# Optimization experiments

Measured on AMD Instinct MI355X. Metric: run time of the kernel, lower is better.

The kernel has to match this reference:

```python
import jax, jax.numpy as jnp
import numpy as np

N = 50000
E = 800000
IN_DIM = 512
H1 = IN_DIM // 2   # 256
H2 = IN_DIM // 4   # 128
D = 8
NP_CAYLEY = D * (D - 1) // 2  # 28


def setup_inputs() -> dict:
    key = jax.random.key(0)
    ks = jax.random.split(key, 10)
    x = jax.random.normal(ks[0], (N, IN_DIM), dtype=jnp.float32)
    edge_index = jax.random.randint(ks[1], (2, E), 0, N, dtype=jnp.int64)
    s1 = 1.0 / np.sqrt(IN_DIM)
    s2 = 1.0 / np.sqrt(H1)
    s3 = 1.0 / np.sqrt(H2)
    W1l = jax.random.uniform(ks[2], (H1, IN_DIM), jnp.float32, -s1, s1)
    b1 = jax.random.uniform(ks[3], (H1,), jnp.float32, -s1, s1)
    W1r = jax.random.uniform(ks[4], (H1, IN_DIM), jnp.float32, -s1, s1)
    W2l = jax.random.uniform(ks[5], (H2, H1), jnp.float32, -s2, s2)
    b2 = jax.random.uniform(ks[6], (H2,), jnp.float32, -s2, s2)
    W2r = jax.random.uniform(ks[7], (H2, H1), jnp.float32, -s2, s2)
    Wp = jax.random.uniform(ks[8], (NP_CAYLEY, H2), jnp.float32, -s3, s3)
    bp = jax.random.uniform(ks[9], (NP_CAYLEY,), jnp.float32, -s3, s3)
    return {"x": x, "edge_index": edge_index,
            "W1l": W1l, "b1": b1, "W1r": W1r,
            "W2l": W2l, "b2": b2, "W2r": W2r,
            "Wp": Wp, "bp": bp}


def _sage_conv(x, src, dst, Wl, bl, Wr):
    # PyG SAGEConv (mean aggr): out = lin_l(mean_{j in N(i)} x_j) + lin_r(x_i)
    msg_sum = jax.ops.segment_sum(x[src], dst, num_segments=N)  # [N, F]
    deg = jax.ops.segment_sum(jnp.ones((src.shape[0],), x.dtype), dst,
                              num_segments=N)
    mean = msg_sum / jnp.maximum(deg, 1.0)[:, None]
    return mean @ Wl.T + bl + x @ Wr.T


def _cayley(params):
    # params: [N, d(d-1)/2] -> skew A, then O = (I - A)^{-1} (I + A)
    iu, ju = jnp.triu_indices(D, k=1)  # row-major i<j matches torch loop order
    n = params.shape[0]
    A = jnp.zeros((n, D, D), params.dtype)
    A = A.at[:, iu, ju].set(params)
    A = A.at[:, ju, iu].set(-params)
    I = jnp.eye(D, dtype=params.dtype)
    return jnp.linalg.solve(I[None] - A, I[None] + A)


def reference(x, edge_index, W1l, b1, W1r, W2l, b2, W2r, Wp, bp):
    src, dst = edge_index[0], edge_index[1]
    h = jax.nn.relu(_sage_conv(x, src, dst, W1l, b1, W1r))
    h = jax.nn.relu(_sage_conv(h, src, dst, W2l, b2, W2r))
    params = h @ Wp.T + bp  # [N, 28]
    return _cayley(params)  # [N, 8, 8]
```

## Files before the change

### kernel.cpp

```cpp
#include <hip/hip_runtime.h>
#include <hip/hip_bf16.h>


#define WS_ALIGN(x) (((x) + 255) & ~size_t(255))

typedef __attribute__((ext_vector_type(8))) short short8;
typedef __attribute__((ext_vector_type(4))) float floatx4;

static __device__ __forceinline__ ushort f2b(float f) {
    unsigned u = __builtin_bit_cast(unsigned, f);
    u = (u + 0x7fffu + ((u >> 16) & 1u)) >> 16;
    return (ushort)u;
}
static __device__ __forceinline__ float b2f(ushort h) {
    unsigned u = ((unsigned)h) << 16;
    return __builtin_bit_cast(float, u);
}
static __device__ __forceinline__ unsigned pk2(float a, float b) {
    return (unsigned)f2b(a) | ((unsigned)f2b(b) << 16);
}


__global__ void hist_kernel(const int* __restrict__ dst, int* __restrict__ deg, int E) {
    int e = blockIdx.x * blockDim.x + threadIdx.x;
    if (e < E) atomicAdd(&deg[dst[e]], 1);
}

__global__ __launch_bounds__(256)
void scan_phase1(const int* __restrict__ deg, int* __restrict__ bsum, int n) {
    __shared__ int red[256];
    const int t = threadIdx.x;
    const int i = blockIdx.x * 1024 + t * 4;
    int s = 0;
    if (i + 4 <= n) {
        int4 v = *reinterpret_cast<const int4*>(&deg[i]);
        s = v.x + v.y + v.z + v.w;
    } else {
        for (int k = i; k < n; ++k) s += deg[k];
    }
    red[t] = s;
    __syncthreads();
#pragma unroll
    for (int off = 128; off > 0; off >>= 1) {
        if (t < off) red[t] += red[t + off];
        __syncthreads();
    }
    if (t == 0) bsum[blockIdx.x] = red[0];
}

__global__ __launch_bounds__(256)
void scan_phase2(int* __restrict__ bsum, int* __restrict__ rowptr, int nb, int n) {
    __shared__ int sh[256];
    const int t = threadIdx.x;
    int orig = (t < nb) ? bsum[t] : 0;
    sh[t] = orig;
    __syncthreads();
#pragma unroll
    for (int off = 1; off < 256; off <<= 1) {
        int v = (t >= off) ? sh[t - off] : 0;
        __syncthreads();
        sh[t] += v;
        __syncthreads();
    }
    if (t < nb) bsum[t] = sh[t] - orig;
    if (t == 255) rowptr[n] = sh[255];
}

__global__ __launch_bounds__(256)
void scan_phase3(const int* __restrict__ deg, const int* __restrict__ bsum,
                 int* __restrict__ rowptr, int n) {
    __shared__ int red[256];
    const int t = threadIdx.x;
    const int i = blockIdx.x * 1024 + t * 4;
    int v0 = 0, v1 = 0, v2 = 0, v3 = 0;
    if (i + 4 <= n) {
        int4 v = *reinterpret_cast<const int4*>(&deg[i]);
        v0 = v.x; v1 = v.y; v2 = v.z; v3 = v.w;
    } else {
        if (i     < n) v0 = deg[i];
        if (i + 1 < n) v1 = deg[i + 1];
        if (i + 2 < n) v2 = deg[i + 2];
        if (i + 3 < n) v3 = deg[i + 3];
    }
    int s = v0 + v1 + v2 + v3;
    red[t] = s;
    __syncthreads();
#pragma unroll
    for (int off = 1; off < 256; off <<= 1) {
        int u = (t >= off) ? red[t - off] : 0;
        __syncthreads();
        red[t] += u;
        __syncthreads();
    }
    int pre = bsum[blockIdx.x] + red[t] - s;
    if (i + 4 <= n) {
        int4 o;
        o.x = pre; o.y = pre + v0; o.z = pre + v0 + v1; o.w = pre + v0 + v1 + v2;
        *reinterpret_cast<int4*>(&rowptr[i]) = o;
    } else {
        if (i     < n) rowptr[i]     = pre;
        if (i + 1 < n) rowptr[i + 1] = pre + v0;
        if (i + 2 < n) rowptr[i + 2] = pre + v0 + v1;
        if (i + 3 < n) rowptr[i + 3] = pre + v0 + v1 + v2;
    }
}

__global__ void scatter_kernel(const int* __restrict__ src, const int* __restrict__ dst,
                               const int* __restrict__ rowptr, int* __restrict__ cursor,
                               int* __restrict__ adj, int E) {
    int e = blockIdx.x * blockDim.x + threadIdx.x;
    if (e < E) {
        int d = dst[e];
        int p = atomicAdd(&cursor[d], 1);
        adj[rowptr[d] + p] = src[e];
    }
}

__global__ void build_wcat(const float* __restrict__ W1l, const float* __restrict__ W1r,
                           const float* __restrict__ W2l, const float* __restrict__ W2r,
                           ushort* __restrict__ Wc1, ushort* __restrict__ Wc2) {
    int idx = blockIdx.x * blockDim.x + threadIdx.x;
    const int n1 = (512 * 512) / 8;
    const int n2 = (256 * 256) / 8;
    const float* src;
    ushort* dst;
    if (idx < n1) {
        int e = idx * 8;
        int row = e >> 9, col = e & 511;
        src = (row < 256) ? &W1l[row * 512 + col] : &W1r[(row - 256) * 512 + col];
        dst = &Wc1[e];
    } else if (idx < n1 + n2) {
        int e = (idx - n1) * 8;
        int row = e >> 8, col = e & 255;
        src = (row < 128) ? &W2l[row * 256 + col] : &W2r[(row - 128) * 256 + col];
        dst = &Wc2[e];
    } else {
        return;
    }
    const float4* s4 = reinterpret_cast<const float4*>(src);
    float4 v0 = s4[0], v1 = s4[1];
    short8 o;
    o[0] = (short)f2b(v0.x); o[1] = (short)f2b(v0.y);
    o[2] = (short)f2b(v0.z); o[3] = (short)f2b(v0.w);
    o[4] = (short)f2b(v1.x); o[5] = (short)f2b(v1.y);
    o[6] = (short)f2b(v1.z); o[7] = (short)f2b(v1.w);
    *reinterpret_cast<short8*>(dst) = o;
}


template <int KT, bool CASTA>
__global__ __launch_bounds__(256, 3)
void gemm_p2(const float* __restrict__ Af, const ushort* __restrict__ Ab,
             const ushort* __restrict__ B,
             ushort* __restrict__ Cl, ushort* __restrict__ Cr,
             int M, int S, int gx) {
    constexpr int nt = KT / 64;
    constexpr int NA = CASTA ? 1 : 2;
    __shared__ ushort As[NA][128 * 64];
    __shared__ ushort Bs[2][128 * 64];

    const int tid  = threadIdx.x;
    const int wave = tid >> 6;
    const int lane = tid & 63;

    const int W = gridDim.x;
    const int q = W >> 3, r = W & 7;
    const int xcd = blockIdx.x & 7, slot = blockIdx.x >> 3;
    const int w = (xcd < r ? xcd * (q + 1) : r * (q + 1) + (xcd - r) * q) + slot;
    const int row0 = (w / gx) * 128;
    const int col0 = (w % gx) * 128;

    const int wm = (wave & 1) * 64;
    const int wn = (wave >> 1) * 64;

    floatx4 acc[4][4];
#pragma unroll
    for (int i = 0; i < 4; ++i)
#pragma unroll
        for (int j = 0; j < 4; ++j)
            acc[i][j] = (floatx4){0.f, 0.f, 0.f, 0.f};

    const int rsub = lane >> 3;
    const int ksw  = ((lane & 7) * 16) ^ (rsub << 4);

    const int ar = tid >> 1, ah = tid & 1;
    int agrow = row0 + ar; if (agrow >= M) agrow = M - 1;
    const float* arow = CASTA ? (Af + (size_t)agrow * KT + ah * 32) : nullptr;
    const int arx = (ar & 7) << 4;
    float4 va[8];

    auto stageB = [&](int t, int buf) {
#pragma unroll
        for (int i = 0; i < 4; ++i) {
            int chunk = wave * 4 + i;
            int rr = chunk * 8 + rsub;
            const char* srcp = (const char*)(B + (size_t)(col0 + rr) * KT + t * 64) + ksw;
            __builtin_amdgcn_global_load_lds(
                (const __attribute__((address_space(1))) unsigned int*)srcp,
                (__attribute__((address_space(3))) unsigned int*)(&Bs[buf][chunk * 512]),
                16, 0, 0);
        }
    };
    auto stageA_dma = [&](int t, int buf) {
#pragma unroll
        for (int i = 0; i < 4; ++i) {
            int chunk = wave * 4 + i;
            int rr = chunk * 8 + rsub;
            int grow = row0 + rr;
            if (grow >= M) grow = M - 1;
            const char* srcp = (const char*)(Ab + (size_t)grow * KT + t * 64) + ksw;
            __builtin_amdgcn_global_load_lds(
                (const __attribute__((address_space(1))) unsigned int*)srcp,
                (__attribute__((address_space(3))) unsigned int*)(&As[buf][chunk * 512]),
                16, 0, 0);
        }
    };
    auto loadA = [&](int t) {
        const float* s = arow + t * 64;
#pragma unroll
        for (int j = 0; j < 8; ++j)
            va[j] = *reinterpret_cast<const float4*>(s + j * 4);
    };
    auto packA = [&]() {
        char* alds = (char*)&As[0][0] + ar * 128;
#pragma unroll
        for (int g = 0; g < 4; ++g) {
            uint4 o = make_uint4(pk2(va[2 * g].x, va[2 * g].y),
                                 pk2(va[2 * g].z, va[2 * g].w),
                                 pk2(va[2 * g + 1].x, va[2 * g + 1].y),
                                 pk2(va[2 * g + 1].z, va[2 * g + 1].w));
            *reinterpret_cast<uint4*>(alds + (((ah * 4 + g) * 16) ^ arx)) = o;
        }
    };

    if constexpr (CASTA) loadA(0);
    stageB(0, 0);
    if constexpr (CASTA) {
        packA();
        if (nt > 1) loadA(1);
    } else {
        stageA_dma(0, 0);
    }
    __syncthreads();

#pragma unroll
    for (int t = 0; t < nt; ++t) {
        const int cur = t & 1, nxt = cur ^ 1;
        if (t + 1 < nt) {
            stageB(t + 1, nxt);
            if constexpr (!CASTA) stageA_dma(t + 1, nxt);
        }
        const char* Al = (const char*)&As[CASTA ? 0 : cur][0];
        const char* Bl = (const char*)&Bs[cur][0];
#pragma unroll
        for (int kk = 0; kk < 2; ++kk) {
            short8 af[4], bf[4];
            const int kb = (kk * 64 + ((lane >> 4) << 4)) ^ ((lane & 7) << 4);
#pragma unroll
            for (int im = 0; im < 4; ++im) {
                int rr = wm + im * 16 + (lane & 15);
                af[im] = *reinterpret_cast<const short8*>(Al + rr * 128 + kb);
            }
#pragma unroll
            for (int in = 0; in < 4; ++in) {
                int rr = wn + in * 16 + (lane & 15);
                bf[in] = *reinterpret_cast<const short8*>(Bl + rr * 128 + kb);
            }
#pragma unroll
            for (int im = 0; im < 4; ++im)
#pragma unroll
                for (int in = 0; in < 4; ++in)
                    acc[im][in] = __builtin_amdgcn_mfma_f32_16x16x32_bf16(
                        af[im], bf[in], acc[im][in], 0, 0, 0);
        }
        __syncthreads();
        if constexpr (CASTA) {
            if (t + 1 < nt) {
                packA();
                if (t + 2 < nt) loadA(t + 2);
                __builtin_amdgcn_sched_barrier(0);
                asm volatile("s_waitcnt lgkmcnt(0)" ::: "memory");
                __builtin_amdgcn_s_barrier();
                __builtin_amdgcn_sched_barrier(0);
            }
        }
    }

    ushort* Cbase = (col0 < S) ? Cl : Cr;
    const int cb = (col0 < S) ? col0 : col0 - S;
#pragma unroll
    for (int im = 0; im < 4; ++im) {
#pragma unroll
        for (int reg = 0; reg < 4; ++reg) {
            int rr = row0 + wm + im * 16 + ((lane >> 4) << 2) + reg;
            if (rr < M) {
                size_t base = (size_t)rr * S + cb + wn + (lane & 15);
#pragma unroll
                for (int in = 0; in < 4; ++in)
                    Cbase[base + in * 16] = f2b(acc[im][in][reg]);
            }
        }
    }
}


template <int LPN>
__global__ __launch_bounds__(256)
void aggregate_bf16(const ushort* __restrict__ Yl, const ushort* __restrict__ Yr,
                    const float* __restrict__ bias,
                    const int* __restrict__ rowptr, const int* __restrict__ adj,
                    ushort* __restrict__ H, int n) {
    constexpr int F = LPN * 8;
    const int grp = threadIdx.x / LPN;
    const int sub = threadIdx.x % LPN;
    const int node = blockIdx.x * (256 / LPN) + grp;
    if (node >= n) return;
    const int c = sub * 8;
    const int start = rowptr[node], end = rowptr[node + 1];

    float acc[8];
#pragma unroll
    for (int v = 0; v < 8; ++v) acc[v] = 0.f;

    int e = start;
    for (; e + 8 <= end; e += 8) {
        short8 rr[8];
#pragma unroll
        for (int u = 0; u < 8; ++u) {
            int s = adj[e + u];
            rr[u] = *reinterpret_cast<const short8*>(&Yl[(size_t)s * F + c]);
        }
#pragma unroll
        for (int v = 0; v < 8; ++v) {
            float t0 = (b2f((ushort)rr[0][v]) + b2f((ushort)rr[1][v])) +
                       (b2f((ushort)rr[2][v]) + b2f((ushort)rr[3][v]));
            float t1 = (b2f((ushort)rr[4][v]) + b2f((ushort)rr[5][v])) +
                       (b2f((ushort)rr[6][v]) + b2f((ushort)rr[7][v]));
            acc[v] += t0 + t1;
        }
    }
    for (; e + 4 <= end; e += 4) {
        int s0 = adj[e + 0], s1 = adj[e + 1], s2 = adj[e + 2], s3 = adj[e + 3];
        short8 r0 = *reinterpret_cast<const short8*>(&Yl[(size_t)s0 * F + c]);
        short8 r1 = *reinterpret_cast<const short8*>(&Yl[(size_t)s1 * F + c]);
        short8 r2 = *reinterpret_cast<const short8*>(&Yl[(size_t)s2 * F + c]);
        short8 r3 = *reinterpret_cast<const short8*>(&Yl[(size_t)s3 * F + c]);
#pragma unroll
        for (int v = 0; v < 8; ++v)
            acc[v] += (b2f((ushort)r0[v]) + b2f((ushort)r1[v])) +
                      (b2f((ushort)r2[v]) + b2f((ushort)r3[v]));
    }
    for (; e < end; ++e) {
        int s = adj[e];
        short8 rr = *reinterpret_cast<const short8*>(&Yl[(size_t)s * F + c]);
#pragma unroll
        for (int v = 0; v < 8; ++v) acc[v] += b2f((ushort)rr[v]);
    }

    const int d = end - start;
    const float inv = 1.0f / (float)(d > 0 ? d : 1);
    short8 sv = *reinterpret_cast<const short8*>(&Yr[(size_t)node * F + c]);
    float4 bv0 = *reinterpret_cast<const float4*>(&bias[c]);
    float4 bv1 = *reinterpret_cast<const float4*>(&bias[c + 4]);
    float bb[8] = {bv0.x, bv0.y, bv0.z, bv0.w, bv1.x, bv1.y, bv1.z, bv1.w};
    short8 o;
#pragma unroll
    for (int v = 0; v < 8; ++v)
        o[v] = (short)f2b(fmaxf(acc[v] * inv + b2f((ushort)sv[v]) + bb[v], 0.f));
    *reinterpret_cast<short8*>(&H[(size_t)node * F + c]) = o;
}


__global__ __launch_bounds__(256)
void params_kernel(const ushort* __restrict__ H2, const float* __restrict__ Wp,
                   const float* __restrict__ bp, float* __restrict__ P, int n) {
    __shared__ float WpS[32 * 132];
    __shared__ float bpS[32];
    for (int t = threadIdx.x; t < 32 * 132; t += 256) WpS[t] = 0.f;
    if (threadIdx.x < 32) bpS[threadIdx.x] = (threadIdx.x < 28) ? bp[threadIdx.x] : 0.f;
    __syncthreads();
    for (int t = threadIdx.x; t < 28 * 128; t += 256) {
        int r = t >> 7, c = t & 127;
        WpS[r * 132 + c] = Wp[t];
    }
    __syncthreads();

    const int node = blockIdx.x * 32 + (threadIdx.x >> 3);
    const int l = threadIdx.x & 7;
    if (node >= n) return;

    short8 h8[16];
    const short8* hp = reinterpret_cast<const short8*>(&H2[(size_t)node * 128]);
#pragma unroll
    for (int q = 0; q < 16; ++q) h8[q] = hp[q];

    float acc0 = bpS[l], acc1 = bpS[l + 8], acc2 = bpS[l + 16], acc3 = bpS[l + 24];
#pragma unroll
    for (int q = 0; q < 32; ++q) {
        float h0 = b2f((ushort)h8[q >> 1][(q & 1) * 4 + 0]);
        float h1 = b2f((ushort)h8[q >> 1][(q & 1) * 4 + 1]);
        float h2 = b2f((ushort)h8[q >> 1][(q & 1) * 4 + 2]);
        float h3 = b2f((ushort)h8[q >> 1][(q & 1) * 4 + 3]);
        float4 w0 = *reinterpret_cast<const float4*>(&WpS[(l +  0) * 132 + 4 * q]);
        float4 w1 = *reinterpret_cast<const float4*>(&WpS[(l +  8) * 132 + 4 * q]);
        float4 w2 = *reinterpret_cast<const float4*>(&WpS[(l + 16) * 132 + 4 * q]);
        float4 w3 = *reinterpret_cast<const float4*>(&WpS[(l + 24) * 132 + 4 * q]);
        acc0 += h0 * w0.x + h1 * w0.y + h2 * w0.z + h3 * w0.w;
        acc1 += h0 * w1.x + h1 * w1.y + h2 * w1.z + h3 * w1.w;
        acc2 += h0 * w2.x + h1 * w2.y + h2 * w2.z + h3 * w2.w;
        acc3 += h0 * w3.x + h1 * w3.y + h2 * w3.z + h3 * w3.w;
    }
    float* pout = &P[(size_t)node * 32];
    pout[l]      = acc0;
    pout[l + 8]  = acc1;
    pout[l + 16] = acc2;
    pout[l + 24] = acc3;
}


__global__ __launch_bounds__(256)
void cayley_kernel(const float* __restrict__ P, float* __restrict__ Out, int n) {
    int i = blockIdx.x * blockDim.x + threadIdx.x;
    if (i >= n) return;
    float p[28];
    const float4* pp = reinterpret_cast<const float4*>(&P[(size_t)i * 32]);
#pragma unroll
    for (int q = 0; q < 7; ++q) {
        float4 v = pp[q];
        p[4 * q + 0] = v.x; p[4 * q + 1] = v.y;
        p[4 * q + 2] = v.z; p[4 * q + 3] = v.w;
    }

    float M_[8][8], B_[8][8];
#pragma unroll
    for (int r = 0; r < 8; ++r)
#pragma unroll
        for (int c = 0; c < 8; ++c) {
            M_[r][c] = (r == c) ? 1.f : 0.f;
            B_[r][c] = (r == c) ? 1.f : 0.f;
        }
    {
        int idx = 0;
#pragma unroll
        for (int r = 0; r < 8; ++r)
#pragma unroll
            for (int c = r + 1; c < 8; ++c) {
                float a = p[idx++];
                M_[r][c] -= a;  M_[c][r] += a;
                B_[r][c] += a;  B_[c][r] -= a;
            }
    }
#pragma unroll
    for (int col = 0; col < 8; ++col) {
        float inv = 1.0f / M_[col][col];
#pragma unroll
        for (int c = 0; c < 8; ++c) { M_[col][c] *= inv; B_[col][c] *= inv; }
#pragma unroll
        for (int r = 0; r < 8; ++r) {
            if (r == col) continue;
            float f = M_[r][col];
#pragma unroll
            for (int c = 0; c < 8; ++c) {
                M_[r][c] -= f * M_[col][c];
                B_[r][c] -= f * B_[col][c];
            }
        }
    }
    float* out = &Out[(size_t)i * 64];
#pragma unroll
    for (int r = 0; r < 8; ++r) {
        float4 o0 = make_float4(B_[r][0], B_[r][1], B_[r][2], B_[r][3]);
        float4 o1 = make_float4(B_[r][4], B_[r][5], B_[r][6], B_[r][7]);
        *reinterpret_cast<float4*>(&out[r * 8 + 0]) = o0;
        *reinterpret_cast<float4*>(&out[r * 8 + 4]) = o1;
    }
}


extern "C" void kernel_launch(void* const* d_in, const int* in_sizes, int n_in,
                              void* d_out, int out_size, void* d_ws, size_t ws_size,
                              hipStream_t stream) {
    const float* x   = (const float*)d_in[0];
    const int*   ei  = (const int*)d_in[1];
    const float* W1l = (const float*)d_in[2];
    const float* b1  = (const float*)d_in[3];
    const float* W1r = (const float*)d_in[4];
    const float* W2l = (const float*)d_in[5];
    const float* b2  = (const float*)d_in[6];
    const float* W2r = (const float*)d_in[7];
    const float* Wp  = (const float*)d_in[8];
    const float* bp  = (const float*)d_in[9];
    float* out = (float*)d_out;

    const int IN_DIM = 512;
    const int N = in_sizes[0] / IN_DIM;
    const int E = in_sizes[1] / 2;

    char* ws = (char*)d_ws;
    size_t off = 0;
    int* deg      = (int*)(ws + off); off = WS_ALIGN(off + (size_t)N * 4);
    int* rowptr   = (int*)(ws + off); off = WS_ALIGN(off + (size_t)(N + 1) * 4);
    int* cursor   = (int*)(ws + off); off = WS_ALIGN(off + (size_t)N * 4);
    int* bsum     = (int*)(ws + off); off = WS_ALIGN(off + (size_t)256 * 4);
    int* adj      = (int*)(ws + off); off = WS_ALIGN(off + (size_t)E * 4);
    ushort* Yl    = (ushort*)(ws + off); off = WS_ALIGN(off + (size_t)N * 256 * 2);
    ushort* Yr    = (ushort*)(ws + off); off = WS_ALIGN(off + (size_t)N * 256 * 2);
    ushort* h1    = (ushort*)(ws + off); off = WS_ALIGN(off + (size_t)N * 256 * 2);
    ushort* zl    = (ushort*)(ws + off); off = WS_ALIGN(off + (size_t)N * 128 * 2);
    ushort* zr    = (ushort*)(ws + off); off = WS_ALIGN(off + (size_t)N * 128 * 2);
    ushort* Wc1   = (ushort*)(ws + off); off = WS_ALIGN(off + (size_t)512 * 512 * 2);
    ushort* Wc2   = (ushort*)(ws + off); off = WS_ALIGN(off + (size_t)256 * 256 * 2);
    float*  Pp    = (float*)(ws + off);  off = WS_ALIGN(off + (size_t)N * 32 * 4);

    const int* src = ei;
    const int* dst = ei + E;

    hipMemsetAsync(deg, 0, (size_t)N * 4, stream);
    hipMemsetAsync(cursor, 0, (size_t)N * 4, stream);

    int eb = (E + 255) / 256;
    int nb = (N + 1023) / 1024;
    hist_kernel<<<eb, 256, 0, stream>>>(dst, deg, E);
    scan_phase1<<<nb, 256, 0, stream>>>(deg, bsum, N);
    scan_phase2<<<1, 256, 0, stream>>>(bsum, rowptr, nb, N);
    scan_phase3<<<nb, 256, 0, stream>>>(deg, bsum, rowptr, N);
    scatter_kernel<<<eb, 256, 0, stream>>>(src, dst, rowptr, cursor, adj, E);

    build_wcat<<<((512 * 512 + 256 * 256) / 8 + 255) / 256, 256, 0, stream>>>(
        W1l, W1r, W2l, W2r, Wc1, Wc2);

    int gm = (N + 127) / 128;

    gemm_p2<512, true><<<gm * 4, 256, 0, stream>>>(
        x, (const ushort*)nullptr, Wc1, Yl, Yr, N, 256, 4);
    aggregate_bf16<32><<<(N + 7) / 8, 256, 0, stream>>>(Yl, Yr, b1, rowptr, adj, h1, N);

    gemm_p2<256, false><<<gm * 2, 256, 0, stream>>>(
        (const float*)nullptr, h1, Wc2, zl, zr, N, 128, 2);
    ushort* h2 = Yl;
    aggregate_bf16<16><<<(N + 15) / 16, 256, 0, stream>>>(zl, zr, b2, rowptr, adj, h2, N);

    params_kernel<<<(N + 31) / 32, 256, 0, stream>>>(h2, Wp, bp, Pp, N);
    cayley_kernel<<<(N + 255) / 256, 256, 0, stream>>>(Pp, out, N);
}
```

Measured before the change: 307.4 us.

## Replace fused-cast pipelined GEMM with separate bf16 cast and simple GEMM

Moves the fp32-to-bf16 conversion of x out of the first GEMM into a standalone cast kernel writing a bf16 copy to workspace. Replaces the templated double-buffered GEMM with a single-buffered bf16 GEMM that stages both A and B via LDS DMA each k-step with full barriers. This simplifies the kernel and register pressure but adds an extra full pass over x and removes load/compute overlap.

```diff
diff --git a/kernel.cpp b/kernel.cpp
--- a/kernel.cpp
+++ b/kernel.cpp
@@ -15,9 +15,6 @@
 static __device__ __forceinline__ float b2f(ushort h) {
     unsigned u = ((unsigned)h) << 16;
     return __builtin_bit_cast(float, u);
-}
-static __device__ __forceinline__ unsigned pk2(float a, float b) {
-    return (unsigned)f2b(a) | ((unsigned)f2b(b) << 16);
 }
 
 
@@ -113,6 +110,20 @@
         int d = dst[e];
         int p = atomicAdd(&cursor[d], 1);
         adj[rowptr[d] + p] = src[e];
+    }
+}
+
+
+__global__ void cast_kernel(const float* __restrict__ src, ushort* __restrict__ dst, int n8) {
+    for (int i = blockIdx.x * blockDim.x + threadIdx.x; i < n8; i += gridDim.x * blockDim.x) {
+        const float4* s4 = reinterpret_cast<const float4*>(src + (size_t)i * 8);
+        float4 v0 = s4[0], v1 = s4[1];
+        short8 o;
+        o[0] = (short)f2b(v0.x); o[1] = (short)f2b(v0.y);
+        o[2] = (short)f2b(v0.z); o[3] = (short)f2b(v0.w);
+        o[4] = (short)f2b(v1.x); o[5] = (short)f2b(v1.y);
+        o[6] = (short)f2b(v1.z); o[7] = (short)f2b(v1.w);
+        *reinterpret_cast<short8*>(dst + (size_t)i * 8) = o;
     }
 }
 
@@ -148,17 +159,12 @@
 }
 
 
-template <int KT, bool CASTA>
-__global__ __launch_bounds__(256, 3)
-void gemm_p2(const float* __restrict__ Af, const ushort* __restrict__ Ab,
-             const ushort* __restrict__ B,
-             ushort* __restrict__ Cl, ushort* __restrict__ Cr,
-             int M, int S, int gx) {
-    constexpr int nt = KT / 64;
-    constexpr int NA = CASTA ? 1 : 2;
-    __shared__ ushort As[NA][128 * 64];
-    __shared__ ushort Bs[2][128 * 64];
-
+__global__ __launch_bounds__(256)
+void gemm_bf16(const ushort* __restrict__ A, const ushort* __restrict__ B,
+               ushort* __restrict__ Cl, ushort* __restrict__ Cr,
+               int M, int K, int S, int gx) {
+    __shared__ ushort As[128 * 64];
+    __shared__ ushort Bs[128 * 64];
     const int tid  = threadIdx.x;
     const int wave = tid >> 6;
     const int lane = tid & 63;
@@ -183,75 +189,32 @@
     const int rsub = lane >> 3;
     const int ksw  = ((lane & 7) * 16) ^ (rsub << 4);
 
-    const int ar = tid >> 1, ah = tid & 1;
-    int agrow = row0 + ar; if (agrow >= M) agrow = M - 1;
-    const float* arow = CASTA ? (Af + (size_t)agrow * KT + ah * 32) : nullptr;
-    const int arx = (ar & 7) << 4;
-    float4 va[8];
-
-    auto stageB = [&](int t, int buf) {
-#pragma unroll
-        for (int i = 0; i < 4; ++i) {
-            int chunk = wave * 4 + i;
-            int rr = chunk * 8 + rsub;
-            const char* srcp = (const char*)(B + (size_t)(col0 + rr) * KT + t * 64) + ksw;
-            __builtin_amdgcn_global_load_lds(
-                (const __attribute__((address_space(1))) unsigned int*)srcp,
-                (__attribute__((address_space(3))) unsigned int*)(&Bs[buf][chunk * 512]),
-                16, 0, 0);
-        }
-    };
-    auto stageA_dma = [&](int t, int buf) {
+    for (int k0 = 0; k0 < K; k0 += 64) {
 #pragma unroll
         for (int i = 0; i < 4; ++i) {
             int chunk = wave * 4 + i;
             int rr = chunk * 8 + rsub;
             int grow = row0 + rr;
             if (grow >= M) grow = M - 1;
-            const char* srcp = (const char*)(Ab + (size_t)grow * KT + t * 64) + ksw;
+            const char* srcp = (const char*)(A + (size_t)grow * K + k0) + ksw;
             __builtin_amdgcn_global_load_lds(
                 (const __attribute__((address_space(1))) unsigned int*)srcp,
-                (__attribute__((address_space(3))) unsigned int*)(&As[buf][chunk * 512]),
+                (__attribute__((address_space(3))) unsigned int*)(&As[chunk * 512]),
                 16, 0, 0);
         }
-    };
-    auto loadA = [&](int t) {
-        const float* s = arow + t * 64;
-#pragma unroll
-        for (int j = 0; j < 8; ++j)
-            va[j] = *reinterpret_cast<const float4*>(s + j * 4);
-    };
-    auto packA = [&]() {
-        char* alds = (char*)&As[0][0] + ar * 128;
-#pragma unroll
-        for (int g = 0; g < 4; ++g) {
-            uint4 o = make_uint4(pk2(va[2 * g].x, va[2 * g].y),
-                                 pk2(va[2 * g].z, va[2 * g].w),
-                                 pk2(va[2 * g + 1].x, va[2 * g + 1].y),
-                                 pk2(va[2 * g + 1].z, va[2 * g + 1].w));
-            *reinterpret_cast<uint4*>(alds + (((ah * 4 + g) * 16) ^ arx)) = o;
-        }
-    };
-
-    if constexpr (CASTA) loadA(0);
-    stageB(0, 0);
-    if constexpr (CASTA) {
-        packA();
-        if (nt > 1) loadA(1);
-    } else {
-        stageA_dma(0, 0);
-    }
-    __syncthreads();
-
-#pragma unroll
-    for (int t = 0; t < nt; ++t) {
-        const int cur = t & 1, nxt = cur ^ 1;
-        if (t + 1 < nt) {
-            stageB(t + 1, nxt);
-            if constexpr (!CASTA) stageA_dma(t + 1, nxt);
-        }
-        const char* Al = (const char*)&As[CASTA ? 0 : cur][0];
-        const char* Bl = (const char*)&Bs[cur][0];
+#pragma unroll
+        for (int i = 0; i < 4; ++i) {
+            int chunk = wave * 4 + i;
+            int rr = chunk * 8 + rsub;
+            int gcol = col0 + rr;
+            const char* srcp = (const char*)(B + (size_t)gcol * K + k0) + ksw;
+            __builtin_amdgcn_global_load_lds(
+                (const __attribute__((address_space(1))) unsigned int*)srcp,
+                (__attribute__((address_space(3))) unsigned int*)(&Bs[chunk * 512]),
+                16, 0, 0);
+        }
+        __syncthreads();
+
 #pragma unroll
         for (int kk = 0; kk < 2; ++kk) {
             short8 af[4], bf[4];
@@ -259,12 +222,12 @@
 #pragma unroll
             for (int im = 0; im < 4; ++im) {
                 int rr = wm + im * 16 + (lane & 15);
-                af[im] = *reinterpret_cast<const short8*>(Al + rr * 128 + kb);
+                af[im] = *reinterpret_cast<const short8*>((const char*)As + rr * 128 + kb);
             }
 #pragma unroll
             for (int in = 0; in < 4; ++in) {
                 int rr = wn + in * 16 + (lane & 15);
-                bf[in] = *reinterpret_cast<const short8*>(Bl + rr * 128 + kb);
+                bf[in] = *reinterpret_cast<const short8*>((const char*)Bs + rr * 128 + kb);
             }
 #pragma unroll
             for (int im = 0; im < 4; ++im)
@@ -274,16 +237,6 @@
                         af[im], bf[in], acc[im][in], 0, 0, 0);
         }
         __syncthreads();
-        if constexpr (CASTA) {
-            if (t + 1 < nt) {
-                packA();
-                if (t + 2 < nt) loadA(t + 2);
-                __builtin_amdgcn_sched_barrier(0);
-                asm volatile("s_waitcnt lgkmcnt(0)" ::: "memory");
-                __builtin_amdgcn_s_barrier();
-                __builtin_amdgcn_sched_barrier(0);
-            }
-        }
     }
 
     ushort* Cbase = (col0 < S) ? Cl : Cr;
@@ -503,6 +456,7 @@
     int* cursor   = (int*)(ws + off); off = WS_ALIGN(off + (size_t)N * 4);
     int* bsum     = (int*)(ws + off); off = WS_ALIGN(off + (size_t)256 * 4);
     int* adj      = (int*)(ws + off); off = WS_ALIGN(off + (size_t)E * 4);
+    ushort* xb    = (ushort*)(ws + off); off = WS_ALIGN(off + (size_t)N * 512 * 2);
     ushort* Yl    = (ushort*)(ws + off); off = WS_ALIGN(off + (size_t)N * 256 * 2);
     ushort* Yr    = (ushort*)(ws + off); off = WS_ALIGN(off + (size_t)N * 256 * 2);
     ushort* h1    = (ushort*)(ws + off); off = WS_ALIGN(off + (size_t)N * 256 * 2);
@@ -526,17 +480,16 @@
     scan_phase3<<<nb, 256, 0, stream>>>(deg, bsum, rowptr, N);
     scatter_kernel<<<eb, 256, 0, stream>>>(src, dst, rowptr, cursor, adj, E);
 
+    cast_kernel<<<2048, 256, 0, stream>>>(x, xb, N * 512 / 8);
     build_wcat<<<((512 * 512 + 256 * 256) / 8 + 255) / 256, 256, 0, stream>>>(
         W1l, W1r, W2l, W2r, Wc1, Wc2);
 
     int gm = (N + 127) / 128;
 
-    gemm_p2<512, true><<<gm * 4, 256, 0, stream>>>(
-        x, (const ushort*)nullptr, Wc1, Yl, Yr, N, 256, 4);
+    gemm_bf16<<<gm * 4, 256, 0, stream>>>(xb, Wc1, Yl, Yr, N, 512, 256, 4);
     aggregate_bf16<32><<<(N + 7) / 8, 256, 0, stream>>>(Yl, Yr, b1, rowptr, adj, h1, N);
 
-    gemm_p2<256, false><<<gm * 2, 256, 0, stream>>>(
-        (const float*)nullptr, h1, Wc2, zl, zr, N, 128, 2);
+    gemm_bf16<<<gm * 2, 256, 0, stream>>>(h1, Wc2, zl, zr, N, 256, 128, 2);
     ushort* h2 = Yl;
     aggregate_bf16<16><<<(N + 15) / 16, 256, 0, stream>>>(zl, zr, b2, rowptr, adj, h2, N);
 
```

New measurement: 298.2 us. 3.0% less time.
